# Optimization experiments

Measured on AMD Instinct MI355X. Metric: run time of the kernel, lower is better.

Reference implementation:

```python
import jax, jax.numpy as jnp
import numpy as np

B, N, DIM, K, H, R = 128, 196, 384, 16, 6, 4  # batch, tokens, channels, bases, heads, adapter ratio


def setup_inputs() -> dict:
    key = jax.random.key(0)
    ks = jax.random.split(key, 4)
    d_r = DIM // R
    return {
        "x": jax.random.normal(ks[0], (B, N, DIM), jnp.float32),
        "W1": jax.random.normal(ks[1], (DIM, d_r), jnp.float32) * 0.02,
        "b1": jnp.zeros((d_r,), jnp.float32),
        "W2": jax.random.normal(ks[2], (d_r, K * H), jnp.float32) * 0.02,
        "b2": jnp.zeros((K * H,), jnp.float32),
        "weight_bank": jax.random.normal(ks[3], (K, N, N), jnp.float32) * 0.02,
    }


def reference(x, W1, b1, W2, b2, weight_bank):
    Bsz, n, C = x.shape
    hdim = C // H
    # adapter MLP: Linear -> GELU(exact/erf, torch default) -> Linear
    hid = jax.nn.gelu(x @ W1 + b1, approximate=False)
    mix = (hid @ W2 + b2).reshape(Bsz, n, K, H)
    # mode='softmax': normalize mixing policy over the k bases
    mix = jax.nn.softmax(mix, axis=2)
    # dynamic per-sample token-mixing matrix [B, n, n, H]
    weight = jnp.einsum('bnkh,knm->bnmh', mix, weight_bank)
    # mix tokens: contract over source token index n
    xh = x.reshape(Bsz, n, H, hdim)
    out = jnp.einsum('bnhc,bnmh->bmhc', xh, weight).reshape(Bsz, n, C)
    return out
```

## Files before the change

kernel.cpp:

```cpp
#include <hip/hip_runtime.h>
#include <math.h>

#define BB  128
#define NN  196
#define CDIM 384
#define KK  16
#define HH  6
#define DR  96
#define HD  64
#define MP  208
#define NCHUNK 7
#define PLANE 6656

typedef __attribute__((ext_vector_type(8))) short bf16x8;
typedef __attribute__((ext_vector_type(4))) float f32x4;

__device__ __forceinline__ unsigned short f2bf(float f) {
    unsigned u = __float_as_uint(f);
    u += 0x7FFFu + ((u >> 16) & 1u);
    return (unsigned short)(u >> 16);
}
__device__ __forceinline__ unsigned pk2bf(float lo, float hi) {
    return (unsigned)f2bf(lo) | ((unsigned)f2bf(hi) << 16);
}

union AFrag { unsigned u[4]; bf16x8 f; };

__global__ __launch_bounds__(256) void prep_kernel(
    const float* __restrict__ W1, const float* __restrict__ W2,
    const float* __restrict__ wb,
    unsigned short* __restrict__ W1T, unsigned short* __restrict__ W2T,
    unsigned short* __restrict__ wbT)
{
    const int bid = blockIdx.x;
    const int t   = threadIdx.x;
    if (bid < DR) {
        const int c = bid;
        for (int k = t; k < CDIM; k += 256)
            W1T[(size_t)c * CDIM + k] = f2bf(W1[(size_t)k * DR + c]);
        if (t < DR)
            W2T[(size_t)c * DR + t] = f2bf(W2[(size_t)t * DR + c]);
    } else {
        const int n = bid - DR;
        const int m = t;
        if (m < MP) {
            unsigned o[8] = {0u, 0u, 0u, 0u, 0u, 0u, 0u, 0u};
            if (n < NN && m < NN) {
                #pragma unroll
                for (int j = 0; j < 8; ++j) {
                    const float a = wb[((size_t)(2 * j)     * NN + n) * NN + m];
                    const float c = wb[((size_t)(2 * j + 1) * NN + n) * NN + m];
                    o[j] = pk2bf(a, c);
                }
            }
            unsigned* dst = (unsigned*)(wbT + ((size_t)n * MP + m) * KK);
            *(uint4*)dst       = make_uint4(o[0], o[1], o[2], o[3]);
            *(uint4*)(dst + 4) = make_uint4(o[4], o[5], o[6], o[7]);
        }
    }
}

__global__ __launch_bounds__(256, 3) void mixa_kernel(
    const float* __restrict__ x,  const unsigned short* __restrict__ W1T,
    const float* __restrict__ b1, const unsigned short* __restrict__ W2T,
    const float* __restrict__ b2, const unsigned short* __restrict__ wbT,
    unsigned short* __restrict__ A)
{
    __shared__ unsigned short hidb[32][104];
    __shared__ unsigned short msc[32][96];

    const int t    = threadIdx.x;
    const int w    = t >> 6;
    const int wm   = w & 1;
    const int wc   = w >> 1;
    const int lane = t & 63;
    const int l15  = lane & 15;
    const int lq   = lane >> 4;
    const int b    = blockIdx.x & 127;
    const int nc   = blockIdx.x >> 7;
    const int n0   = nc * 32;

    f32x4 acc[3];
    #pragma unroll
    for (int ct = 0; ct < 3; ++ct) {
        const float bj = b1[wc * 48 + ct * 16 + l15];
        acc[ct] = (f32x4){bj, bj, bj, bj};
    }
    const int nrow = n0 + wm * 16 + l15;
    const bool rv  = (nrow < NN);
    const float* xrow = x + ((size_t)b * NN + nrow) * CDIM;
    for (int kc = 0; kc < CDIM; kc += 32) {
        float4 u = make_float4(0.f, 0.f, 0.f, 0.f);
        float4 v = make_float4(0.f, 0.f, 0.f, 0.f);
        if (rv) {
            u = *(const float4*)(xrow + kc + 8 * lq);
            v = *(const float4*)(xrow + kc + 8 * lq + 4);
        }
        AFrag af;
        af.u[0] = pk2bf(u.x, u.y); af.u[1] = pk2bf(u.z, u.w);
        af.u[2] = pk2bf(v.x, v.y); af.u[3] = pk2bf(v.z, v.w);
        #pragma unroll
        for (int ct = 0; ct < 3; ++ct) {
            const bf16x8 bf = *(const bf16x8*)(W1T + (size_t)(wc * 48 + ct * 16 + l15) * CDIM + kc + 8 * lq);
            acc[ct] = __builtin_amdgcn_mfma_f32_16x16x32_bf16(af.f, bf, acc[ct], 0, 0, 0);
        }
    }
    #pragma unroll
    for (int ct = 0; ct < 3; ++ct)
        #pragma unroll
        for (int r = 0; r < 4; ++r) {
            const float vv = acc[ct][r];
            hidb[wm * 16 + lq * 4 + r][wc * 48 + ct * 16 + l15] =
                f2bf(0.5f * vv * (1.0f + erff(vv * 0.70710678118654752f)));
        }
    __syncthreads();

    f32x4 acc2[3];
    #pragma unroll
    for (int ct = 0; ct < 3; ++ct) {
        const float bj = b2[wc * 48 + ct * 16 + l15];
        acc2[ct] = (f32x4){bj, bj, bj, bj};
    }
    #pragma unroll
    for (int kc = 0; kc < DR; kc += 32) {
        const bf16x8 af = *(const bf16x8*)&hidb[wm * 16 + l15][kc + 8 * lq];
        #pragma unroll
        for (int ct = 0; ct < 3; ++ct) {
            const bf16x8 bf = *(const bf16x8*)(W2T + (size_t)(wc * 48 + ct * 16 + l15) * DR + kc + 8 * lq);
            acc2[ct] = __builtin_amdgcn_mfma_f32_16x16x32_bf16(af, bf, acc2[ct], 0, 0, 0);
        }
    }
    __syncthreads();

    #pragma unroll
    for (int ct = 0; ct < 3; ++ct)
        #pragma unroll
        for (int r = 0; r < 4; ++r)
            hidb[wm * 16 + lq * 4 + r][wc * 48 + ct * 16 + l15] = f2bf(acc2[ct][r]);
    __syncthreads();

    if (t < 192) {
        const int r = t / 6, h = t - r * 6;
        float lg[KK];
        float mx = -1e30f;
        #pragma unroll
        for (int k = 0; k < KK; ++k) {
            lg[k] = __uint_as_float((unsigned)hidb[r][6 * k + h] << 16);
            mx = fmaxf(mx, lg[k]);
        }
        float s = 0.f;
        #pragma unroll
        for (int k = 0; k < KK; ++k) { lg[k] = __expf(lg[k] - mx); s += lg[k]; }
        const float inv = 1.0f / s;
        unsigned o[8];
        #pragma unroll
        for (int jj = 0; jj < 8; ++jj)
            o[jj] = pk2bf(lg[2 * jj] * inv, lg[2 * jj + 1] * inv);
        unsigned* op = (unsigned*)&msc[r][16 * h];
        *(uint4*)op       = make_uint4(o[0], o[1], o[2], o[3]);
        *(uint4*)(op + 4) = make_uint4(o[4], o[5], o[6], o[7]);
    }
    __syncthreads();

    const bf16x8 z8 = {0, 0, 0, 0, 0, 0, 0, 0};
    const f32x4  cz = {0.f, 0.f, 0.f, 0.f};
    const size_t bc6 = ((size_t)b * NCHUNK + nc) * HH;

    for (int i = 0; i < 8; ++i) {
        const int nl = 4 * i + w;
        const int n  = n0 + nl;
        bf16x8 af = z8;
        if (l15 < HH && lq < 2)
            af = *(const bf16x8*)&msc[nl][l15 * 16 + 8 * lq];
        f32x4 c[13];
        #pragma unroll
        for (int mt = 0; mt < 13; ++mt) {
            bf16x8 bf = z8;
            if (lq < 2)
                bf = *(const bf16x8*)(wbT + ((size_t)n * MP + mt * 16 + l15) * KK + 8 * lq);
            c[mt] = __builtin_amdgcn_mfma_f32_16x16x32_bf16(af, bf, cz, 0, 0, 0);
        }
        if (lq < 2) {
            unsigned short* p0 = A + (bc6 + (size_t)(lq * 4)) * PLANE + (size_t)nl * MP + l15;
            #pragma unroll
            for (int mt = 0; mt < 13; ++mt) {
                p0[mt * 16]         = f2bf(c[mt][0]);
                p0[mt * 16 + PLANE] = f2bf(c[mt][1]);
            }
            if (lq == 0) {
                #pragma unroll
                for (int mt = 0; mt < 13; ++mt) {
                    p0[mt * 16 + 2 * PLANE] = f2bf(c[mt][2]);
                    p0[mt * 16 + 3 * PLANE] = f2bf(c[mt][3]);
                }
            }
        }
    }
}

__global__ __launch_bounds__(192, 3) void mix_gemm_kernel(
    const float* __restrict__ x, const unsigned short* __restrict__ Ab,
    float* __restrict__ out)
{
    __shared__ unsigned short xT[192][40];
    __shared__ unsigned short As[3][32][68];

    const int t    = threadIdx.x;
    const int bid  = blockIdx.x;
    const int b    = bid & 127;
    const int sub  = bid >> 7;
    const int q    = sub >> 1;
    const int hp   = sub & 1;
    const int m0   = q * 52;
    const int qvalid = (q == 3) ? 40 : 52;
    const int lw   = t >> 6;
    const int hbase = hp * 3;
    const int lane = t & 63;
    const int l15  = lane & 15;
    const int lq   = lane >> 4;
    const int c0   = hp * 192;

    const f32x4 cz = {0.f, 0.f, 0.f, 0.f};
    f32x4 acc[4][4];
    #pragma unroll
    for (int mt = 0; mt < 4; ++mt)
        #pragma unroll
        for (int ct = 0; ct < 4; ++ct) acc[mt][ct] = cz;

    unsigned long long av[8];

    {
        const size_t bc6 = (size_t)b * NCHUNK * HH + hbase;
        #pragma unroll
        for (int i = 0; i < 8; ++i) {
            const int P = t + 192 * i;
            const int row = P >> 4, p = P & 15;
            av[i] = *(const unsigned long long*)(
                Ab + (bc6 + (size_t)(row >> 5)) * PLANE + (size_t)(row & 31) * MP + m0 + 4 * p);
        }
    }

    for (int nc = 0; nc < NCHUNK; ++nc) {
        const int n0 = nc * 32;
        if (nc) __syncthreads();

        #pragma unroll
        for (int i = 0; i < 8; ++i) {
            const int P = t + 192 * i;
            const int row = P >> 4, p = P & 15;
            *(unsigned long long*)&As[row >> 5][row & 31][4 * p] = av[i];
        }

        #pragma unroll
        for (int it = 0; it < 4; ++it) {
            const int task = t + 192 * it;
            const int p  = task & 15;
            const int cq = task >> 4;
            const int n  = n0 + 2 * p;
            float4 va = make_float4(0.f, 0.f, 0.f, 0.f);
            float4 vb = make_float4(0.f, 0.f, 0.f, 0.f);
            if (n < NN)     va = *(const float4*)(x + ((size_t)b * NN + n) * CDIM + c0 + 4 * cq);
            if (n + 1 < NN) vb = *(const float4*)(x + ((size_t)b * NN + n + 1) * CDIM + c0 + 4 * cq);
            *(unsigned*)&xT[4 * cq + 0][2 * p] = pk2bf(va.x, vb.x);
            *(unsigned*)&xT[4 * cq + 1][2 * p] = pk2bf(va.y, vb.y);
            *(unsigned*)&xT[4 * cq + 2][2 * p] = pk2bf(va.z, vb.z);
            *(unsigned*)&xT[4 * cq + 3][2 * p] = pk2bf(va.w, vb.w);
        }
        __syncthreads();

        if (nc + 1 < NCHUNK) {
            const size_t bc6 = ((size_t)b * NCHUNK + nc + 1) * HH + hbase;
            #pragma unroll
            for (int i = 0; i < 8; ++i) {
                const int P = t + 192 * i;
                const int row = P >> 4, p = P & 15;
                av[i] = *(const unsigned long long*)(
                    Ab + (bc6 + (size_t)(row >> 5)) * PLANE + (size_t)(row & 31) * MP + m0 + 4 * p);
            }
        }

        bf16x8 afr[4], bfr[4];
        #pragma unroll
        for (int mt = 0; mt < 4; ++mt) {
            union { unsigned short s[8]; bf16x8 v; } u;
            #pragma unroll
            for (int j = 0; j < 8; ++j)
                u.s[j] = As[lw][8 * lq + j][mt * 16 + l15];
            afr[mt] = u.v;
        }
        #pragma unroll
        for (int ct = 0; ct < 4; ++ct)
            bfr[ct] = *(const bf16x8*)&xT[lw * 64 + ct * 16 + l15][8 * lq];
        #pragma unroll
        for (int mt = 0; mt < 4; ++mt)
            #pragma unroll
            for (int ct = 0; ct < 4; ++ct)
                acc[mt][ct] = __builtin_amdgcn_mfma_f32_16x16x32_bf16(
                    afr[mt], bfr[ct], acc[mt][ct], 0, 0, 0);
    }

    const int h = hbase + lw;
    #pragma unroll
    for (int mt = 0; mt < 4; ++mt) {
        #pragma unroll
        for (int r = 0; r < 4; ++r) {
            const int ms = mt * 16 + lq * 4 + r;
            if (ms < qvalid) {
                float* op = out + ((size_t)b * NN + m0 + ms) * CDIM + h * HD + l15;
                #pragma unroll
                for (int ct = 0; ct < 4; ++ct)
                    op[ct * 16] = acc[mt][ct][r];
            }
        }
    }
}

__global__ __launch_bounds__(128, 3) void adapter_kernel(
    const float* __restrict__ x,   const unsigned short* __restrict__ W1T,
    const float* __restrict__ b1,  const unsigned short* __restrict__ W2T,
    const float* __restrict__ b2,  unsigned short* __restrict__ mix_out)
{
    __shared__ unsigned short hidb[16][104];

    const int t    = threadIdx.x;
    const int wc   = t >> 6;
    const int lane = t & 63;
    const int l15  = lane & 15;
    const int lq   = lane >> 4;
    const int row0 = blockIdx.x * 16;

    f32x4 acc[3];
    #pragma unroll
    for (int ct = 0; ct < 3; ++ct) {
        const float bj = b1[wc * 48 + ct * 16 + l15];
        acc[ct] = (f32x4){bj, bj, bj, bj};
    }
    const float* xrow = x + (size_t)(row0 + l15) * CDIM;
    for (int kc = 0; kc < CDIM; kc += 32) {
        const float4 u = *(const float4*)(xrow + kc + 8 * lq);
        const float4 v = *(const float4*)(xrow + kc + 8 * lq + 4);
        AFrag af;
        af.u[0] = pk2bf(u.x, u.y); af.u[1] = pk2bf(u.z, u.w);
        af.u[2] = pk2bf(v.x, v.y); af.u[3] = pk2bf(v.z, v.w);
        #pragma unroll
        for (int ct = 0; ct < 3; ++ct) {
            const bf16x8 bf = *(const bf16x8*)(W1T + (size_t)(wc * 48 + ct * 16 + l15) * CDIM + kc + 8 * lq);
            acc[ct] = __builtin_amdgcn_mfma_f32_16x16x32_bf16(af.f, bf, acc[ct], 0, 0, 0);
        }
    }
    #pragma unroll
    for (int ct = 0; ct < 3; ++ct)
        #pragma unroll
        for (int r = 0; r < 4; ++r) {
            const float vv = acc[ct][r];
            hidb[lq * 4 + r][wc * 48 + ct * 16 + l15] =
                f2bf(0.5f * vv * (1.0f + erff(vv * 0.70710678118654752f)));
        }
    __syncthreads();

    f32x4 acc2[3];
    #pragma unroll
    for (int ct = 0; ct < 3; ++ct) {
        const float bj = b2[wc * 48 + ct * 16 + l15];
        acc2[ct] = (f32x4){bj, bj, bj, bj};
    }
    #pragma unroll
    for (int kc = 0; kc < DR; kc += 32) {
        const bf16x8 af = *(const bf16x8*)&hidb[l15][kc + 8 * lq];
        #pragma unroll
        for (int ct = 0; ct < 3; ++ct) {
            const bf16x8 bf = *(const bf16x8*)(W2T + (size_t)(wc * 48 + ct * 16 + l15) * DR + kc + 8 * lq);
            acc2[ct] = __builtin_amdgcn_mfma_f32_16x16x32_bf16(af, bf, acc2[ct], 0, 0, 0);
        }
    }
    __syncthreads();

    #pragma unroll
    for (int ct = 0; ct < 3; ++ct)
        #pragma unroll
        for (int r = 0; r < 4; ++r)
            hidb[lq * 4 + r][wc * 48 + ct * 16 + l15] = f2bf(acc2[ct][r]);
    __syncthreads();

    if (t < 96) {
        const int r = t / 6, h = t % 6;
        float lg[KK];
        float mx = -1e30f;
        #pragma unroll
        for (int k = 0; k < KK; ++k) {
            lg[k] = __uint_as_float((unsigned)hidb[r][6 * k + h] << 16);
            mx = fmaxf(mx, lg[k]);
        }
        float s = 0.f;
        #pragma unroll
        for (int k = 0; k < KK; ++k) { lg[k] = __expf(lg[k] - mx); s += lg[k]; }
        const float inv = 1.0f / s;
        unsigned o[8];
        #pragma unroll
        for (int jj = 0; jj < 8; ++jj)
            o[jj] = pk2bf(lg[2 * jj] * inv, lg[2 * jj + 1] * inv);
        unsigned* op = (unsigned*)(mix_out + ((size_t)(row0 + r) * HH + h) * KK);
        *(uint4*)op       = make_uint4(o[0], o[1], o[2], o[3]);
        *(uint4*)(op + 4) = make_uint4(o[4], o[5], o[6], o[7]);
    }
}

__global__ __launch_bounds__(192, 3) void mix_mfma_fb_kernel(
    const float* __restrict__ x,  const unsigned short* __restrict__ mixb,
    const unsigned short* __restrict__ wbT, float* __restrict__ out)
{
    __shared__ unsigned short xT[192][40];
    __shared__ unsigned short Asb[3][64][40];

    const int t    = threadIdx.x;
    const int bid  = blockIdx.x;
    const int b    = bid & 127;
    const int sub  = bid >> 7;
    const int q    = sub >> 1;
    const int hp   = sub & 1;
    const int m0   = q * 52;
    const int qvalid = (q == 3) ? 40 : 52;
    const int lw   = t >> 6;
    const int hbase = hp * 3;
    const int lane = t & 63;
    const int l15  = lane & 15;
    const int lq   = lane >> 4;
    const int c0   = hp * 192;

    const bf16x8 z8 = {0, 0, 0, 0, 0, 0, 0, 0};
    const f32x4  cz = {0.f, 0.f, 0.f, 0.f};

    f32x4 acc[4][4];
    #pragma unroll
    for (int mt = 0; mt < 4; ++mt)
        #pragma unroll
        for (int ct = 0; ct < 4; ++ct) acc[mt][ct] = cz;

    for (int nc = 0; nc < 7; ++nc) {
        const int n0 = nc * 32;
        __syncthreads();

        #pragma unroll
        for (int it = 0; it < 4; ++it) {
            const int task = t + 192 * it;
            const int p  = task & 15;
            const int cq = task >> 4;
            const int n  = n0 + 2 * p;
            float4 va = make_float4(0.f, 0.f, 0.f, 0.f);
            float4 vb = make_float4(0.f, 0.f, 0.f, 0.f);
            if (n < NN)     va = *(const float4*)(x + ((size_t)b * NN + n) * CDIM + c0 + 4 * cq);
            if (n + 1 < NN) vb = *(const float4*)(x + ((size_t)b * NN + n + 1) * CDIM + c0 + 4 * cq);
            *(unsigned*)&xT[4 * cq + 0][2 * p] = pk2bf(va.x, vb.x);
            *(unsigned*)&xT[4 * cq + 1][2 * p] = pk2bf(va.y, vb.y);
            *(unsigned*)&xT[4 * cq + 2][2 * p] = pk2bf(va.z, vb.z);
            *(unsigned*)&xT[4 * cq + 3][2 * p] = pk2bf(va.w, vb.w);
        }

        for (int nl = lw; nl < 32; nl += 3) {
            const int n = n0 + nl;
            if (n < NN) {
                bf16x8 af = z8;
                if (l15 < HH && lq < 2)
                    af = *(const bf16x8*)(mixb + (((size_t)b * NN + n) * HH + l15) * KK + 8 * lq);
                #pragma unroll
                for (int mt = 0; mt < 4; ++mt) {
                    const int m = m0 + mt * 16 + l15;
                    bf16x8 bf = z8;
                    if (lq < 2 && m < NN)
                        bf = *(const bf16x8*)(wbT + ((size_t)n * MP + m) * KK + 8 * lq);
                    const f32x4 c = __builtin_amdgcn_mfma_f32_16x16x32_bf16(af, bf, cz, 0, 0, 0);
                    #pragma unroll
                    for (int r = 0; r < 4; ++r) {
                        const int hh = lq * 4 + r;
                        if (hh >= hbase && hh < hbase + 3)
                            Asb[hh - hbase][mt * 16 + l15][nl] = f2bf(c[r]);
                    }
                }
            } else {
                #pragma unroll
                for (int mt = 0; mt < 4; ++mt)
                    #pragma unroll
                    for (int r = 0; r < 4; ++r) {
                        const int hh = lq * 4 + r;
                        if (hh >= hbase && hh < hbase + 3)
                            Asb[hh - hbase][mt * 16 + l15][nl] = 0;
                    }
            }
        }
        __syncthreads();

        bf16x8 afr[4], bfr[4];
        #pragma unroll
        for (int mt = 0; mt < 4; ++mt)
            afr[mt] = *(const bf16x8*)&Asb[lw][mt * 16 + l15][8 * lq];
        #pragma unroll
        for (int ct = 0; ct < 4; ++ct)
            bfr[ct] = *(const bf16x8*)&xT[lw * 64 + ct * 16 + l15][8 * lq];
        #pragma unroll
        for (int mt = 0; mt < 4; ++mt)
            #pragma unroll
            for (int ct = 0; ct < 4; ++ct)
                acc[mt][ct] = __builtin_amdgcn_mfma_f32_16x16x32_bf16(
                    afr[mt], bfr[ct], acc[mt][ct], 0, 0, 0);
    }

    const int h = hbase + lw;
    #pragma unroll
    for (int mt = 0; mt < 4; ++mt) {
        #pragma unroll
        for (int r = 0; r < 4; ++r) {
            const int ms = mt * 16 + lq * 4 + r;
            if (ms < qvalid) {
                float* op = out + ((size_t)b * NN + m0 + ms) * CDIM + h * HD + l15;
                #pragma unroll
                for (int ct = 0; ct < 4; ++ct)
                    op[ct * 16] = acc[mt][ct][r];
            }
        }
    }
}

extern "C" void kernel_launch(void* const* d_in, const int* in_sizes, int n_in,
                              void* d_out, int out_size, void* d_ws, size_t ws_size,
                              hipStream_t stream) {
    (void)in_sizes; (void)n_in; (void)out_size;
    const float* x  = (const float*)d_in[0];
    const float* W1 = (const float*)d_in[1];
    const float* b1 = (const float*)d_in[2];
    const float* W2 = (const float*)d_in[3];
    const float* b2 = (const float*)d_in[4];
    const float* wb = (const float*)d_in[5];
    float* out = (float*)d_out;

    const size_t W1T_OFF  = 0;
    const size_t W2T_OFF  = 73728;
    const size_t WBT_OFF  = 92160;
    const size_t A_OFF    = 1583104;
    const size_t NEED     = A_OFF + 71565312ull + 1024ull;

    unsigned short* w1t = (unsigned short*)((char*)d_ws + W1T_OFF);
    unsigned short* w2t = (unsigned short*)((char*)d_ws + W2T_OFF);
    unsigned short* wbt = (unsigned short*)((char*)d_ws + WBT_OFF);

    prep_kernel<<<DR + 224, 256, 0, stream>>>(W1, W2, wb, w1t, w2t, wbt);

    if (ws_size >= NEED) {
        unsigned short* Ab = (unsigned short*)((char*)d_ws + A_OFF);
        mixa_kernel<<<BB * NCHUNK, 256, 0, stream>>>(x, w1t, b1, w2t, b2, wbt, Ab);
        mix_gemm_kernel<<<8 * BB, 192, 0, stream>>>(x, Ab, out);
    } else {
        unsigned short* mixbuf = (unsigned short*)((char*)d_ws + A_OFF);
        adapter_kernel<<<(BB * NN) / 16, 128, 0, stream>>>(x, w1t, b1, w2t, b2, mixbuf);
        mix_mfma_fb_kernel<<<8 * BB, 192, 0, stream>>>(x, mixbuf, wbt, out);
    }
}
```

Measured before the change: 191.1 us.

## Prefetch x and weight-bank fragments, swap MFMA operands for packed stores

The adapter GEMM loop now loads the next x chunk before converting and multiplying the current one, which hides global load latency. The token-mixing build stage double-buffers weight-bank fragments across two register sets (ta/tb), so loads for the next token row overlap the MFMAs of the current one. The MFMA operands are swapped so each lane holds four contiguous m outputs for one head. That allows 8-byte packed bf16 stores instead of scattered 2-byte stores. The cost is higher register pressure from 26 bf16x8 buffers, which could reduce occupancy.

Result: no change. 191.8 us (+0.4%).

```diff
diff --git a/kernel.cpp b/kernel.cpp
--- a/kernel.cpp
+++ b/kernel.cpp
@@ -89,12 +89,18 @@
     const int nrow = n0 + wm * 16 + l15;
     const bool rv  = (nrow < NN);
     const float* xrow = x + ((size_t)b * NN + nrow) * CDIM;
+    float4 u = make_float4(0.f, 0.f, 0.f, 0.f);
+    float4 v = make_float4(0.f, 0.f, 0.f, 0.f);
+    if (rv) {
+        u = *(const float4*)(xrow + 8 * lq);
+        v = *(const float4*)(xrow + 8 * lq + 4);
+    }
     for (int kc = 0; kc < CDIM; kc += 32) {
-        float4 u = make_float4(0.f, 0.f, 0.f, 0.f);
-        float4 v = make_float4(0.f, 0.f, 0.f, 0.f);
-        if (rv) {
-            u = *(const float4*)(xrow + kc + 8 * lq);
-            v = *(const float4*)(xrow + kc + 8 * lq + 4);
+        float4 un = make_float4(0.f, 0.f, 0.f, 0.f);
+        float4 vn = make_float4(0.f, 0.f, 0.f, 0.f);
+        if (rv && kc + 32 < CDIM) {
+            un = *(const float4*)(xrow + kc + 32 + 8 * lq);
+            vn = *(const float4*)(xrow + kc + 32 + 8 * lq + 4);
         }
         AFrag af;
         af.u[0] = pk2bf(u.x, u.y); af.u[1] = pk2bf(u.z, u.w);
@@ -104,6 +110,7 @@
             const bf16x8 bf = *(const bf16x8*)(W1T + (size_t)(wc * 48 + ct * 16 + l15) * CDIM + kc + 8 * lq);
             acc[ct] = __builtin_amdgcn_mfma_f32_16x16x32_bf16(af.f, bf, acc[ct], 0, 0, 0);
         }
+        u = un; v = vn;
     }
     #pragma unroll
     for (int ct = 0; ct < 3; ++ct)
@@ -165,33 +172,56 @@
     const bf16x8 z8 = {0, 0, 0, 0, 0, 0, 0, 0};
     const f32x4  cz = {0.f, 0.f, 0.f, 0.f};
     const size_t bc6 = ((size_t)b * NCHUNK + nc) * HH;
-
-    for (int i = 0; i < 8; ++i) {
-        const int nl = 4 * i + w;
-        const int n  = n0 + nl;
-        bf16x8 af = z8;
-        if (l15 < HH && lq < 2)
-            af = *(const bf16x8*)&msc[nl][l15 * 16 + 8 * lq];
-        f32x4 c[13];
-        #pragma unroll
-        for (int mt = 0; mt < 13; ++mt) {
-            bf16x8 bf = z8;
-            if (lq < 2)
-                bf = *(const bf16x8*)(wbT + ((size_t)n * MP + mt * 16 + l15) * KK + 8 * lq);
-            c[mt] = __builtin_amdgcn_mfma_f32_16x16x32_bf16(af, bf, cz, 0, 0, 0);
-        }
-        if (lq < 2) {
-            unsigned short* p0 = A + (bc6 + (size_t)(lq * 4)) * PLANE + (size_t)nl * MP + l15;
+    const bool kv = (lq < 2);
+    const bool hv = (l15 < HH);
+
+    bf16x8 ta[13], tb[13];
+    {
+        const unsigned short* wp = wbT + ((size_t)(n0 + w) * MP + l15) * KK + 8 * lq;
+        #pragma unroll
+        for (int mt = 0; mt < 13; ++mt)
+            ta[mt] = kv ? *(const bf16x8*)(wp + (size_t)(mt * 16) * KK) : z8;
+    }
+
+    #pragma unroll
+    for (int ii = 0; ii < 4; ++ii) {
+        {
+            const int nl = 8 * ii + w;
+            const bf16x8 bmix = (hv && kv)
+                ? *(const bf16x8*)&msc[nl][l15 * 16 + 8 * lq] : z8;
+            {
+                const unsigned short* wp = wbT + ((size_t)(n0 + nl + 4) * MP + l15) * KK + 8 * lq;
+                #pragma unroll
+                for (int mt = 0; mt < 13; ++mt)
+                    tb[mt] = kv ? *(const bf16x8*)(wp + (size_t)(mt * 16) * KK) : z8;
+            }
+            unsigned short* p0 = A + (bc6 + l15) * PLANE + (size_t)nl * MP + lq * 4;
             #pragma unroll
             for (int mt = 0; mt < 13; ++mt) {
-                p0[mt * 16]         = f2bf(c[mt][0]);
-                p0[mt * 16 + PLANE] = f2bf(c[mt][1]);
-            }
-            if (lq == 0) {
-                #pragma unroll
-                for (int mt = 0; mt < 13; ++mt) {
-                    p0[mt * 16 + 2 * PLANE] = f2bf(c[mt][2]);
-                    p0[mt * 16 + 3 * PLANE] = f2bf(c[mt][3]);
+                const f32x4 c = __builtin_amdgcn_mfma_f32_16x16x32_bf16(ta[mt], bmix, cz, 0, 0, 0);
+                if (hv) {
+                    *(uint2*)(p0 + mt * 16) =
+                        make_uint2(pk2bf(c[0], c[1]), pk2bf(c[2], c[3]));
+                }
+            }
+        }
+        {
+            const int nl = 8 * ii + w + 4;
+            const bf16x8 bmix = (hv && kv)
+                ? *(const bf16x8*)&msc[nl][l15 * 16 + 8 * lq] : z8;
+            if (ii < 3) {
+                const unsigned short* wp = wbT + ((size_t)(n0 + nl + 4) * MP + l15) * KK + 8 * lq;
+                #pragma unroll
+                for (int mt = 0; mt < 13; ++mt)
+                    ta[mt] = kv ? *(const bf16x8*)(wp + (size_t)(mt * 16) * KK) : z8;
+            }
+            unsigned short* p0 = A + (bc6 + l15) * PLANE + (size_t)nl * MP + lq * 4;
+            #pragma unroll
+            for (int mt = 0; mt < 13; ++mt) {
+                const f32x4 c = __builtin_amdgcn_mfma_f32_16x16x32_bf16(tb[mt], bmix, cz, 0, 0, 0);
+                if (hv) {
+                    *(uint2*)(p0 + mt * 16) =
+                        make_uint2(pk2bf(c[0], c[1]), pk2bf(c[2], c[3]));
                 }
             }
         }
```
